# Kernel optimization log

Hardware: AMD Instinct MI355X
Metric: run time of the kernel (lower is better)

The kernel has to match this reference:

```python
import jax, jax.numpy as jnp
import numpy as np

BN_EPS = 1e-5


def _interpolate(xyz1, xyz2, points2):
    # squared pairwise distances [B, N, S]
    d = (jnp.sum(xyz1 ** 2, -1)[:, :, None]
         + jnp.sum(xyz2 ** 2, -1)[:, None, :]
         - 2.0 * jnp.einsum('bnc,bsc->bns', xyz1, xyz2))
    # 3 smallest distances (torch does a full sort; top-3 is the same math)
    neg_d, idx = jax.lax.top_k(-d, 3)          # [B, N, 3]
    dists = -neg_d
    w = 1.0 / (dists + 1e-8)
    w = w / jnp.sum(w, -1, keepdims=True)
    # gather points2 features at idx: [B, N, 3, D]
    gathered = jnp.take_along_axis(points2[:, None, :, :],
                                   idx[:, :, :, None], axis=2)
    return jnp.sum(gathered * w[:, :, :, None], axis=2)  # [B, N, D]


def _conv_bn_relu(x, w, b, gamma, beta):
    # x: [B, N, Cin]; 1x1 Conv1d == per-point dense layer
    y = jnp.einsum('bnc,oc->bno', x, w) + b
    mean = jnp.mean(y, axis=(0, 1))
    var = jnp.mean((y - mean) ** 2, axis=(0, 1))  # biased var (torch BN training)
    y = (y - mean) * jax.lax.rsqrt(var + BN_EPS) * gamma + beta
    return jax.nn.relu(y)


def setup_inputs() -> dict:
    key = jax.random.key(0)
    ks = jax.random.split(key, 8)
    B, N, S, D1, D2 = 8, 8192, 2048, 128, 256
    in_ch, mlp = D1 + D2, [256, 128]
    inp = {
        'xyz1': jax.random.normal(ks[0], (B, N, 3), jnp.float32),
        'xyz2': jax.random.normal(ks[1], (B, S, 3), jnp.float32),
        'points1': jax.random.normal(ks[2], (B, N, D1), jnp.float32),
        'points2': jax.random.normal(ks[3], (B, S, D2), jnp.float32),
    }
    c = in_ch
    for i, o in enumerate(mlp):
        kw = jax.random.fold_in(ks[4], i)
        inp[f'w{i}'] = jax.random.normal(kw, (o, c), jnp.float32) * (1.0 / np.sqrt(c))
        inp[f'b{i}'] = jnp.zeros((o,), jnp.float32)
        inp[f'g{i}'] = jnp.ones((o,), jnp.float32)
        inp[f'beta{i}'] = jnp.zeros((o,), jnp.float32)
        c = o
    return inp


def reference(xyz1, xyz2, points1, points2,
              w0, b0, g0, beta0, w1, b1, g1, beta1):
    interp = _interpolate(xyz1, xyz2, points2)          # [B, N, D2]
    x = jnp.concatenate([points1, interp], axis=-1)     # [B, N, D1+D2]
    x = _conv_bn_relu(x, w0, b0, g0, beta0)
    x = _conv_bn_relu(x, w1, b1, g1, beta1)
    return x                                            # [B, N, mlp[-1]]
```

## Files before the change

### kernel.cpp

```cpp
#include <hip/hip_runtime.h>
#include <hip/hip_bf16.h>

#define BATCH 8
#define NPTS  8192
#define SPTS  2048
#define D1C   128
#define D2C   256
#define C_IN  384
#define O0    256
#define O1    128
#define MROWS (BATCH * NPTS)
#define NCHUNK 8
#define CHSZ   256

typedef __attribute__((ext_vector_type(8))) short short8v;
typedef __attribute__((ext_vector_type(4))) float f32x4;

__device__ __forceinline__ unsigned short f2bf(float f) {
    union { float f; unsigned u; } v; v.f = f;
    unsigned u = v.u;
    return (unsigned short)((u + 0x7fffu + ((u >> 16) & 1u)) >> 16);
}
__device__ __forceinline__ float bf2f(unsigned short h) {
    union { unsigned u; float f; } v; v.u = ((unsigned)h) << 16;
    return v.f;
}
__device__ __forceinline__ void gload_lds16(const void* g, void* l) {
    __builtin_amdgcn_global_load_lds(
        (const __attribute__((address_space(1))) void*)g,
        (__attribute__((address_space(3))) void*)l, 16, 0, 0);
}

__global__ __launch_bounds__(256, 8) void nn3_scan(
    const float* __restrict__ xyz1, const float* __restrict__ xyz2,
    float* __restrict__ candD, int* __restrict__ candI)
{
    __shared__ float4 P[CHSZ];
    const int t  = threadIdx.x;
    const int qb = blockIdx.x;
    const int c  = blockIdx.y;
    const int b  = qb >> 5;

    {
        const float* src = xyz2 + ((size_t)b * SPTS + c * CHSZ) * 3;
        float px = src[t * 3 + 0];
        float py = src[t * 3 + 1];
        float pz = src[t * 3 + 2];
        P[t] = make_float4(px, py, pz, px * px + py * py + pz * pz);
    }
    __syncthreads();

    const int q = qb * 256 + t;
    const float* qp = xyz1 + (size_t)q * 3;
    const float qx = qp[0], qy = qp[1], qz = qp[2];
    const float qn = qx * qx + qy * qy + qz * qz;

    float d0 = 1e30f, d1 = 1e30f, d2 = 1e30f;
    int   i0 = 0,     i1 = 0,     i2 = 0;
    const int gbase = c * CHSZ;

    #pragma unroll 4
    for (int s = 0; s < CHSZ; ++s) {
        float4 p = P[s];
        float dot = qx * p.x + qy * p.y + qz * p.z;
        float d = (qn + p.w) - 2.0f * dot;
        bool c0 = d < d0, c1 = d < d1, c2 = d < d2;
        int gi = gbase + s;
        float t2 = __builtin_amdgcn_fmed3f(d, d1, d2);
        float t1 = __builtin_amdgcn_fmed3f(d, d0, d1);
        i2 = c1 ? i1 : (c2 ? gi : i2);
        i1 = c0 ? i0 : (c1 ? gi : i1);
        i0 = c0 ? gi : i0;
        d2 = t2; d1 = t1; d0 = fminf(d, d0);
    }

    const size_t base = (size_t)c * (MROWS * 3) + (size_t)q * 3;
    candD[base + 0] = d0; candD[base + 1] = d1; candD[base + 2] = d2;
    candI[base + 0] = i0; candI[base + 1] = i1; candI[base + 2] = i2;
}

__global__ __launch_bounds__(256) void nn3_merge(
    const float* __restrict__ candD, const int* __restrict__ candI,
    int* __restrict__ idx3, float* __restrict__ wgt3)
{
    const int q = blockIdx.x * 256 + threadIdx.x;

    float d0 = 1e30f, d1 = 1e30f, d2 = 1e30f;
    int   i0 = 0,     i1 = 0,     i2 = 0;

    #pragma unroll
    for (int c = 0; c < NCHUNK; ++c) {
        const size_t base = (size_t)c * (MROWS * 3) + (size_t)q * 3;
        #pragma unroll
        for (int j = 0; j < 3; ++j) {
            float d = candD[base + j];
            int  gi = candI[base + j];
            bool c0 = d < d0, c1 = d < d1, c2 = d < d2;
            float t2 = __builtin_amdgcn_fmed3f(d, d1, d2);
            float t1 = __builtin_amdgcn_fmed3f(d, d0, d1);
            i2 = c1 ? i1 : (c2 ? gi : i2);
            i1 = c0 ? i0 : (c1 ? gi : i1);
            i0 = c0 ? gi : i0;
            d2 = t2; d1 = t1; d0 = fminf(d, d0);
        }
    }

    float wa = 1.0f / (d0 + 1e-8f);
    float wb = 1.0f / (d1 + 1e-8f);
    float wc = 1.0f / (d2 + 1e-8f);
    float inv = 1.0f / (wa + wb + wc);
    wa *= inv; wb *= inv; wc *= inv;

    idx3[q * 3 + 0] = i0;
    idx3[q * 3 + 1] = i1;
    idx3[q * 3 + 2] = i2;
    wgt3[q * 3 + 0] = wa;
    wgt3[q * 3 + 1] = wb;
    wgt3[q * 3 + 2] = wc;
}

__global__ __launch_bounds__(256) void cvt_f32_bf16(
    const float* __restrict__ src, unsigned short* __restrict__ dst)
{
    int i = blockIdx.x * 256 + threadIdx.x;
    float4 v = ((const float4*)src)[i];
    ushort4 o;
    o.x = f2bf(v.x); o.y = f2bf(v.y); o.z = f2bf(v.z); o.w = f2bf(v.w);
    ((ushort4*)dst)[i] = o;
}

__global__ __launch_bounds__(256) void interp_kernel(
    const float* __restrict__ points2,
    const int* __restrict__ idx3, const float* __restrict__ wgt3,
    unsigned short* __restrict__ xI)
{
    const int w    = threadIdx.x >> 6;
    const int lane = threadIdx.x & 63;
    const int m    = blockIdx.x * 4 + w;
    const int b    = m >> 13;

    const float* p2b = points2 + (size_t)b * SPTS * D2C;
    const int  gi0 = idx3[m * 3 + 0];
    const int  gi1 = idx3[m * 3 + 1];
    const int  gi2 = idx3[m * 3 + 2];
    const float w0 = wgt3[m * 3 + 0];
    const float w1 = wgt3[m * 3 + 1];
    const float w2 = wgt3[m * 3 + 2];

    float4 a = *(const float4*)(p2b + (size_t)gi0 * D2C + lane * 4);
    float4 bb = *(const float4*)(p2b + (size_t)gi1 * D2C + lane * 4);
    float4 c = *(const float4*)(p2b + (size_t)gi2 * D2C + lane * 4);

    ushort4 o;
    o.x = f2bf(w0 * a.x + w1 * bb.x + w2 * c.x);
    o.y = f2bf(w0 * a.y + w1 * bb.y + w2 * c.y);
    o.z = f2bf(w0 * a.z + w1 * bb.z + w2 * c.z);
    o.w = f2bf(w0 * a.w + w1 * bb.w + w2 * c.w);
    *(ushort4*)(xI + (size_t)m * D2C + lane * 4) = o;
}

__global__ __launch_bounds__(512) void gemm0_mfma(
    const float* __restrict__ points1, const unsigned short* __restrict__ xI,
    const unsigned short* __restrict__ w0bf, const float* __restrict__ b0,
    unsigned short* __restrict__ y0bf,
    float* __restrict__ sum0, float* __restrict__ sq0)
{
    __shared__ __align__(16) unsigned short As[128 * 32];
    __shared__ __align__(16) unsigned short Bs[256 * 32];

    const int t    = threadIdx.x;
    const int lane = t & 63;
    const int w    = t >> 6;
    const int wm   = w >> 2;
    const int wn   = w & 3;
    const int rowBase = blockIdx.x * 128;

    const int r      = t >> 2;
    const int ks_log = (t & 3) ^ ((t >> 3) & 3);

    const float* p1row = points1 + (size_t)(rowBase + r) * D1C;
    const unsigned short* xrow = xI + (size_t)(rowBase + r) * D2C + ks_log * 8;
    unsigned short* asw = As + t * 8;
    char* ldsA = (char*)As + w * 1024;

    const unsigned short* gB0 = w0bf + (size_t)r * C_IN + ks_log * 8;
    const unsigned short* gB1 = w0bf + (size_t)(128 + r) * C_IN + ks_log * 8;
    char* ldsB0 = (char*)Bs + w * 1024;
    char* ldsB1 = (char*)Bs + 8192 + w * 1024;

    const int rp = (lane & 15) * 64 + (((lane >> 4) ^ ((lane >> 1) & 3)) * 16);
    const char* aBase = (const char*)As + (wm * 64) * 64 + rp;
    const char* bBase = (const char*)Bs + (wn * 64) * 64 + rp;

    f32x4 acc[4][4] = {};

    for (int kt = 0; kt < C_IN / 32; ++kt) {
        gload_lds16(gB0 + kt * 32, ldsB0);
        gload_lds16(gB1 + kt * 32, ldsB1);

        if (kt < 4) {
            const int k = kt * 32 + ks_log * 8;
            float4 f0 = *(const float4*)(p1row + k);
            float4 f1 = *(const float4*)(p1row + k + 4);
            short8v av;
            av[0] = (short)f2bf(f0.x); av[1] = (short)f2bf(f0.y);
            av[2] = (short)f2bf(f0.z); av[3] = (short)f2bf(f0.w);
            av[4] = (short)f2bf(f1.x); av[5] = (short)f2bf(f1.y);
            av[6] = (short)f2bf(f1.z); av[7] = (short)f2bf(f1.w);
            *(short8v*)asw = av;
        } else {
            gload_lds16(xrow + (kt - 4) * 32, ldsA);
        }

        __syncthreads();

        short8v a[4], bf[4];
        #pragma unroll
        for (int m = 0; m < 4; ++m) a[m]  = *(const short8v*)(aBase + m * 1024);
        #pragma unroll
        for (int n = 0; n < 4; ++n) bf[n] = *(const short8v*)(bBase + n * 1024);
        #pragma unroll
        for (int m = 0; m < 4; ++m)
            #pragma unroll
            for (int n = 0; n < 4; ++n)
                acc[m][n] = __builtin_amdgcn_mfma_f32_16x16x32_bf16(
                    a[m], bf[n], acc[m][n], 0, 0, 0);

        __syncthreads();
    }

    const int colw = wn * 64 + (lane & 15);
    const int rowE = rowBase + wm * 64 + ((lane >> 4) * 4);
    float bias[4];
    #pragma unroll
    for (int n = 0; n < 4; ++n) bias[n] = b0[colw + n * 16];

    float cs[4] = {0.f, 0.f, 0.f, 0.f}, cq[4] = {0.f, 0.f, 0.f, 0.f};
    #pragma unroll
    for (int m = 0; m < 4; ++m)
        #pragma unroll
        for (int n = 0; n < 4; ++n)
            #pragma unroll
            for (int j = 0; j < 4; ++j) {
                float v = acc[m][n][j] + bias[n];
                y0bf[(size_t)(rowE + m * 16 + j) * O0 + colw + n * 16] = f2bf(v);
                cs[n] += v; cq[n] += v * v;
            }

    #pragma unroll
    for (int n = 0; n < 4; ++n) {
        float s = cs[n], qv = cq[n];
        s  += __shfl_xor(s, 16);  s  += __shfl_xor(s, 32);
        qv += __shfl_xor(qv, 16); qv += __shfl_xor(qv, 32);
        if (lane < 16) {
            atomicAdd(&sum0[colw + n * 16], s);
            atomicAdd(&sq0[colw + n * 16], qv);
        }
    }
}

__global__ void stats_kernel(const float* __restrict__ sum, const float* __restrict__ sq,
                             const float* __restrict__ g, const float* __restrict__ beta,
                             float* __restrict__ scale, float* __restrict__ shift,
                             int C, float invM)
{
    int c = blockIdx.x * blockDim.x + threadIdx.x;
    if (c < C) {
        float mean = sum[c] * invM;
        float var  = sq[c] * invM - mean * mean;
        float s = g[c] * rsqrtf(var + 1e-5f);
        scale[c] = s;
        shift[c] = beta[c] - mean * s;
    }
}

__global__ __launch_bounds__(256) void gemm1_mfma(
    const unsigned short* __restrict__ x1, const unsigned short* __restrict__ w1bf,
    const float* __restrict__ scale0, const float* __restrict__ shift0,
    const float* __restrict__ b1, float* __restrict__ out,
    float* __restrict__ sum1, float* __restrict__ sq1)
{
    __shared__ __align__(16) unsigned short As[128 * 32];
    __shared__ __align__(16) unsigned short Bs[128 * 32];
    __shared__ float sc[O0], sh[O0];

    const int t    = threadIdx.x;
    const int lane = t & 63;
    const int w    = t >> 6;
    const int wm   = w >> 1, wn = w & 1;
    const int rowBase = blockIdx.x * 128;

    sc[t] = scale0[t];
    sh[t] = shift0[t];
    __syncthreads();

    const int r      = t >> 2;
    const int kl     = t & 3;
    const int kp     = kl ^ ((r >> 1) & 3);
    const int ks_log = kl ^ ((r >> 1) & 3);

    const unsigned short* gA0 = x1 + (size_t)(rowBase + r) * O0 + kl * 8;
    const unsigned short* gA1 = x1 + (size_t)(rowBase + 64 + r) * O0 + kl * 8;
    unsigned short* dA0 = As + r * 32 + kp * 8;
    unsigned short* dA1 = As + (64 + r) * 32 + kp * 8;

    const unsigned short* gB0 = w1bf + (size_t)r * O0 + ks_log * 8;
    const unsigned short* gB1 = w1bf + (size_t)(64 + r) * O0 + ks_log * 8;
    char* ldsB0 = (char*)Bs + w * 1024;
    char* ldsB1 = (char*)Bs + 4096 + w * 1024;

    const int rp = (lane & 15) * 64 + (((lane >> 4) ^ ((lane >> 1) & 3)) * 16);
    const char* aBase = (const char*)As + (wm * 64) * 64 + rp;
    const char* bBase = (const char*)Bs + (wn * 64) * 64 + rp;

    f32x4 acc[4][4] = {};

    for (int kt = 0; kt < O0 / 32; ++kt) {
        gload_lds16(gB0 + kt * 32, ldsB0);
        gload_lds16(gB1 + kt * 32, ldsB1);

        const int ch = kt * 32 + kl * 8;
        float4 s0v = *(const float4*)(sc + ch);
        float4 s1v = *(const float4*)(sc + ch + 4);
        float4 h0v = *(const float4*)(sh + ch);
        float4 h1v = *(const float4*)(sh + ch + 4);
        short8v v0 = *(const short8v*)(gA0 + kt * 32);
        short8v v1 = *(const short8v*)(gA1 + kt * 32);
        short8v o0, o1;
        o0[0] = (short)f2bf(fmaxf(0.f, bf2f((unsigned short)v0[0]) * s0v.x + h0v.x));
        o0[1] = (short)f2bf(fmaxf(0.f, bf2f((unsigned short)v0[1]) * s0v.y + h0v.y));
        o0[2] = (short)f2bf(fmaxf(0.f, bf2f((unsigned short)v0[2]) * s0v.z + h0v.z));
        o0[3] = (short)f2bf(fmaxf(0.f, bf2f((unsigned short)v0[3]) * s0v.w + h0v.w));
        o0[4] = (short)f2bf(fmaxf(0.f, bf2f((unsigned short)v0[4]) * s1v.x + h1v.x));
        o0[5] = (short)f2bf(fmaxf(0.f, bf2f((unsigned short)v0[5]) * s1v.y + h1v.y));
        o0[6] = (short)f2bf(fmaxf(0.f, bf2f((unsigned short)v0[6]) * s1v.z + h1v.z));
        o0[7] = (short)f2bf(fmaxf(0.f, bf2f((unsigned short)v0[7]) * s1v.w + h1v.w));
        o1[0] = (short)f2bf(fmaxf(0.f, bf2f((unsigned short)v1[0]) * s0v.x + h0v.x));
        o1[1] = (short)f2bf(fmaxf(0.f, bf2f((unsigned short)v1[1]) * s0v.y + h0v.y));
        o1[2] = (short)f2bf(fmaxf(0.f, bf2f((unsigned short)v1[2]) * s0v.z + h0v.z));
        o1[3] = (short)f2bf(fmaxf(0.f, bf2f((unsigned short)v1[3]) * s0v.w + h0v.w));
        o1[4] = (short)f2bf(fmaxf(0.f, bf2f((unsigned short)v1[4]) * s1v.x + h1v.x));
        o1[5] = (short)f2bf(fmaxf(0.f, bf2f((unsigned short)v1[5]) * s1v.y + h1v.y));
        o1[6] = (short)f2bf(fmaxf(0.f, bf2f((unsigned short)v1[6]) * s1v.z + h1v.z));
        o1[7] = (short)f2bf(fmaxf(0.f, bf2f((unsigned short)v1[7]) * s1v.w + h1v.w));
        *(short8v*)dA0 = o0;
        *(short8v*)dA1 = o1;

        __syncthreads();

        short8v a[4], bf[4];
        #pragma unroll
        for (int m = 0; m < 4; ++m) a[m]  = *(const short8v*)(aBase + m * 1024);
        #pragma unroll
        for (int n = 0; n < 4; ++n) bf[n] = *(const short8v*)(bBase + n * 1024);
        #pragma unroll
        for (int m = 0; m < 4; ++m)
            #pragma unroll
            for (int n = 0; n < 4; ++n)
                acc[m][n] = __builtin_amdgcn_mfma_f32_16x16x32_bf16(
                    a[m], bf[n], acc[m][n], 0, 0, 0);

        __syncthreads();
    }

    const int colw = wn * 64 + (lane & 15);
    const int rowE = rowBase + wm * 64 + ((lane >> 4) * 4);
    float bias[4];
    #pragma unroll
    for (int n = 0; n < 4; ++n) bias[n] = b1[colw + n * 16];

    float cs[4] = {0.f, 0.f, 0.f, 0.f}, cq[4] = {0.f, 0.f, 0.f, 0.f};
    #pragma unroll
    for (int m = 0; m < 4; ++m)
        #pragma unroll
        for (int n = 0; n < 4; ++n)
            #pragma unroll
            for (int j = 0; j < 4; ++j) {
                float v = acc[m][n][j] + bias[n];
                out[(size_t)(rowE + m * 16 + j) * O1 + colw + n * 16] = v;
                cs[n] += v; cq[n] += v * v;
            }

    #pragma unroll
    for (int n = 0; n < 4; ++n) {
        float s = cs[n], qv = cq[n];
        s  += __shfl_xor(s, 16);  s  += __shfl_xor(s, 32);
        qv += __shfl_xor(qv, 16); qv += __shfl_xor(qv, 32);
        if (lane < 16) {
            atomicAdd(&sum1[colw + n * 16], s);
            atomicAdd(&sq1[colw + n * 16], qv);
        }
    }
}

__global__ __launch_bounds__(256) void bn_relu_kernel(
    float* __restrict__ out,
    const float* __restrict__ scale, const float* __restrict__ shift)
{
    int i = blockIdx.x * blockDim.x + threadIdx.x;
    float4 v = ((float4*)out)[i];
    int c = (i * 4) & (O1 - 1);
    v.x = fmaxf(0.f, v.x * scale[c + 0] + shift[c + 0]);
    v.y = fmaxf(0.f, v.y * scale[c + 1] + shift[c + 1]);
    v.z = fmaxf(0.f, v.z * scale[c + 2] + shift[c + 2]);
    v.w = fmaxf(0.f, v.w * scale[c + 3] + shift[c + 3]);
    ((float4*)out)[i] = v;
}

extern "C" void kernel_launch(void* const* d_in, const int* in_sizes, int n_in,
                              void* d_out, int out_size, void* d_ws, size_t ws_size,
                              hipStream_t stream)
{
    const float* xyz1    = (const float*)d_in[0];
    const float* xyz2    = (const float*)d_in[1];
    const float* points1 = (const float*)d_in[2];
    const float* points2 = (const float*)d_in[3];
    const float* w0      = (const float*)d_in[4];
    const float* b0      = (const float*)d_in[5];
    const float* g0      = (const float*)d_in[6];
    const float* beta0   = (const float*)d_in[7];
    const float* w1      = (const float*)d_in[8];
    const float* b1      = (const float*)d_in[9];
    const float* g1      = (const float*)d_in[10];
    const float* beta1   = (const float*)d_in[11];

    float* wsf = (float*)d_ws;
    float* sum0   = wsf;
    float* sq0    = wsf + 256;
    float* sum1   = wsf + 512;
    float* sq1    = wsf + 640;
    float* scale0 = wsf + 768;
    float* shift0 = wsf + 1024;
    float* scale1 = wsf + 1280;
    float* shift1 = wsf + 1408;
    unsigned short* w0bf = (unsigned short*)(wsf + 1536);
    unsigned short* w1bf = (unsigned short*)(wsf + 50688);
    unsigned short* y0bf = (unsigned short*)(wsf + 67072);
    int*   idx3   = (int*)(wsf + 67072);
    float* wgt3   = wsf + 263680;
    float* candD  = wsf + 460288;
    int*   candI  = (int*)(wsf + 2033152);
    unsigned short* xI = (unsigned short*)(wsf + 8455680);

    hipMemsetAsync(d_ws, 0, 768 * sizeof(float), stream);

    cvt_f32_bf16<<<(O0 * C_IN / 4) / 256, 256, 0, stream>>>(w0, w0bf);
    cvt_f32_bf16<<<(O1 * O0 / 4) / 256, 256, 0, stream>>>(w1, w1bf);

    nn3_scan<<<dim3(MROWS / 256, NCHUNK), 256, 0, stream>>>(xyz1, xyz2, candD, candI);
    nn3_merge<<<MROWS / 256, 256, 0, stream>>>(candD, candI, idx3, wgt3);

    interp_kernel<<<MROWS / 4, 256, 0, stream>>>(points2, idx3, wgt3, xI);

    gemm0_mfma<<<MROWS / 128, 512, 0, stream>>>(
        points1, xI, w0bf, b0, y0bf, sum0, sq0);

    stats_kernel<<<1, 256, 0, stream>>>(sum0, sq0, g0, beta0, scale0, shift0,
                                        O0, 1.0f / MROWS);

    gemm1_mfma<<<MROWS / 128, 256, 0, stream>>>(
        y0bf, w1bf, scale0, shift0, b1, (float*)d_out, sum1, sq1);

    stats_kernel<<<1, 128, 0, stream>>>(sum1, sq1, g1, beta1, scale1, shift1,
                                        O1, 1.0f / MROWS);

    bn_relu_kernel<<<(out_size / 4) / 256, 256, 0, stream>>>(
        (float*)d_out, scale1, shift1);
}
```

Before: 196.2 us.

## Precompute padded xyz2 in global, scan without LDS, store gemm1 output as bf16

A small prep kernel turns xyz2 into float4 records (x, y, z, |p|^2) in global memory. The nearest-neighbour scan now reads these directly, which removes the LDS staging and block barrier, and its loop is unrolled by 8 instead of 4. The second GEMM writes a bf16 intermediate instead of the fp32 output, and the final BN+ReLU pass reads that bf16 buffer and writes fp32, halving the traffic of the intermediate read and write. The risks are broadcast global loads in the scan hot loop instead of LDS reads, an extra launch, and bf16 rounding before normalisation.

```diff
diff --git a/kernel.cpp b/kernel.cpp
--- a/kernel.cpp
+++ b/kernel.cpp
@@ -31,24 +31,26 @@
         (__attribute__((address_space(3))) void*)l, 16, 0, 0);
 }
 
+__global__ __launch_bounds__(256) void prep_p4(
+    const float* __restrict__ xyz2, float4* __restrict__ P4g)
+{
+    int i = blockIdx.x * 256 + threadIdx.x;
+    float px = xyz2[i * 3 + 0];
+    float py = xyz2[i * 3 + 1];
+    float pz = xyz2[i * 3 + 2];
+    P4g[i] = make_float4(px, py, pz, px * px + py * py + pz * pz);
+}
+
 __global__ __launch_bounds__(256, 8) void nn3_scan(
-    const float* __restrict__ xyz1, const float* __restrict__ xyz2,
+    const float* __restrict__ xyz1, const float4* __restrict__ P4g,
     float* __restrict__ candD, int* __restrict__ candI)
 {
-    __shared__ float4 P[CHSZ];
     const int t  = threadIdx.x;
     const int qb = blockIdx.x;
     const int c  = blockIdx.y;
     const int b  = qb >> 5;
 
-    {
-        const float* src = xyz2 + ((size_t)b * SPTS + c * CHSZ) * 3;
-        float px = src[t * 3 + 0];
-        float py = src[t * 3 + 1];
-        float pz = src[t * 3 + 2];
-        P[t] = make_float4(px, py, pz, px * px + py * py + pz * pz);
-    }
-    __syncthreads();
+    const float4* __restrict__ P = P4g + ((size_t)b * SPTS + c * CHSZ);
 
     const int q = qb * 256 + t;
     const float* qp = xyz1 + (size_t)q * 3;
@@ -59,7 +61,7 @@
     int   i0 = 0,     i1 = 0,     i2 = 0;
     const int gbase = c * CHSZ;
 
-    #pragma unroll 4
+    #pragma unroll 8
     for (int s = 0; s < CHSZ; ++s) {
         float4 p = P[s];
         float dot = qx * p.x + qy * p.y + qz * p.z;
@@ -277,7 +279,7 @@
 __global__ __launch_bounds__(256) void gemm1_mfma(
     const unsigned short* __restrict__ x1, const unsigned short* __restrict__ w1bf,
     const float* __restrict__ scale0, const float* __restrict__ shift0,
-    const float* __restrict__ b1, float* __restrict__ out,
+    const float* __restrict__ b1, unsigned short* __restrict__ y1bf,
     float* __restrict__ sum1, float* __restrict__ sq1)
 {
     __shared__ __align__(16) unsigned short As[128 * 32];
@@ -377,7 +379,7 @@
             #pragma unroll
             for (int j = 0; j < 4; ++j) {
                 float v = acc[m][n][j] + bias[n];
-                out[(size_t)(rowE + m * 16 + j) * O1 + colw + n * 16] = v;
+                y1bf[(size_t)(rowE + m * 16 + j) * O1 + colw + n * 16] = f2bf(v);
                 cs[n] += v; cq[n] += v * v;
             }
 
@@ -393,18 +395,28 @@
     }
 }
 
-__global__ __launch_bounds__(256) void bn_relu_kernel(
-    float* __restrict__ out,
+__global__ __launch_bounds__(256) void bn_relu_out(
+    const unsigned short* __restrict__ y1bf, float* __restrict__ out,
     const float* __restrict__ scale, const float* __restrict__ shift)
 {
-    int i = blockIdx.x * blockDim.x + threadIdx.x;
-    float4 v = ((float4*)out)[i];
-    int c = (i * 4) & (O1 - 1);
-    v.x = fmaxf(0.f, v.x * scale[c + 0] + shift[c + 0]);
-    v.y = fmaxf(0.f, v.y * scale[c + 1] + shift[c + 1]);
-    v.z = fmaxf(0.f, v.z * scale[c + 2] + shift[c + 2]);
-    v.w = fmaxf(0.f, v.w * scale[c + 3] + shift[c + 3]);
-    ((float4*)out)[i] = v;
+    int i = blockIdx.x * 256 + threadIdx.x;
+    short8v v = ((const short8v*)y1bf)[i];
+    int c = (i * 8) & (O1 - 1);
+    float4 sa = *(const float4*)(scale + c);
+    float4 sb = *(const float4*)(scale + c + 4);
+    float4 ha = *(const float4*)(shift + c);
+    float4 hb = *(const float4*)(shift + c + 4);
+    float4 o0, o1;
+    o0.x = fmaxf(0.f, bf2f((unsigned short)v[0]) * sa.x + ha.x);
+    o0.y = fmaxf(0.f, bf2f((unsigned short)v[1]) * sa.y + ha.y);
+    o0.z = fmaxf(0.f, bf2f((unsigned short)v[2]) * sa.z + ha.z);
+    o0.w = fmaxf(0.f, bf2f((unsigned short)v[3]) * sa.w + ha.w);
+    o1.x = fmaxf(0.f, bf2f((unsigned short)v[4]) * sb.x + hb.x);
+    o1.y = fmaxf(0.f, bf2f((unsigned short)v[5]) * sb.y + hb.y);
+    o1.z = fmaxf(0.f, bf2f((unsigned short)v[6]) * sb.z + hb.z);
+    o1.w = fmaxf(0.f, bf2f((unsigned short)v[7]) * sb.w + hb.w);
+    ((float4*)out)[i * 2 + 0] = o0;
+    ((float4*)out)[i * 2 + 1] = o1;
 }
 
 extern "C" void kernel_launch(void* const* d_in, const int* in_sizes, int n_in,
@@ -435,19 +447,23 @@
     float* shift1 = wsf + 1408;
     unsigned short* w0bf = (unsigned short*)(wsf + 1536);
     unsigned short* w1bf = (unsigned short*)(wsf + 50688);
+    float4* P4g   = (float4*)(wsf + 67072);
+    float*  candD = wsf + 132608;
+    int*    candI = (int*)(wsf + 1705472);
+    int*    idx3  = (int*)(wsf + 3278336);
+    float*  wgt3  = wsf + 3474944;
     unsigned short* y0bf = (unsigned short*)(wsf + 67072);
-    int*   idx3   = (int*)(wsf + 67072);
-    float* wgt3   = wsf + 263680;
-    float* candD  = wsf + 460288;
-    int*   candI  = (int*)(wsf + 2033152);
-    unsigned short* xI = (unsigned short*)(wsf + 8455680);
+    unsigned short* xI   = (unsigned short*)(wsf + 8455680);
+    unsigned short* y1bf = (unsigned short*)(wsf + 8455680);
 
     hipMemsetAsync(d_ws, 0, 768 * sizeof(float), stream);
 
     cvt_f32_bf16<<<(O0 * C_IN / 4) / 256, 256, 0, stream>>>(w0, w0bf);
     cvt_f32_bf16<<<(O1 * O0 / 4) / 256, 256, 0, stream>>>(w1, w1bf);
 
-    nn3_scan<<<dim3(MROWS / 256, NCHUNK), 256, 0, stream>>>(xyz1, xyz2, candD, candI);
+    prep_p4<<<(BATCH * SPTS) / 256, 256, 0, stream>>>(xyz2, P4g);
+
+    nn3_scan<<<dim3(MROWS / 256, NCHUNK), 256, 0, stream>>>(xyz1, P4g, candD, candI);
     nn3_merge<<<MROWS / 256, 256, 0, stream>>>(candD, candI, idx3, wgt3);
 
     interp_kernel<<<MROWS / 4, 256, 0, stream>>>(points2, idx3, wgt3, xI);
@@ -459,11 +475,11 @@
                                         O0, 1.0f / MROWS);
 
     gemm1_mfma<<<MROWS / 128, 256, 0, stream>>>(
-        y0bf, w1bf, scale0, shift0, b1, (float*)d_out, sum1, sq1);
+        y0bf, w1bf, scale0, shift0, b1, y1bf, sum1, sq1);
 
     stats_kernel<<<1, 128, 0, stream>>>(sum1, sq1, g1, beta1, scale1, shift1,
                                         O1, 1.0f / MROWS);
 
-    bn_relu_kernel<<<(out_size / 4) / 256, 256, 0, stream>>>(
-        (float*)d_out, scale1, shift1);
-}
+    bn_relu_out<<<(MROWS * O1 / 8) / 256, 256, 0, stream>>>(
+        y1bf, (float*)d_out, scale1, shift1);
+}
```

After: 202.1 us. 3.0% more time.

## Fuse BatchNorm stats and apply into GEMM epilogues via grid-wide barrier

Applied to the files above, without the earlier changes.

Both GEMM kernels now hold their accumulators in registers, wait at a software grid barrier until every block has added its column sums, then compute the BN scale and shift and write normalized, ReLU'd outputs directly. This removes the two stats kernels and the separate bn_relu pass, drops the fp32 round-trip of the final output, and lets gemm1 stream its already-normalized A operand straight into LDS with global_load_lds. The scheme relies on all 512 blocks being co-resident, which the launch bounds are meant to guarantee; otherwise the spin barrier deadlocks. It also adds spin-wait cost and register pressure from keeping accumulators live across the barrier.

```diff
diff --git a/kernel.cpp b/kernel.cpp
--- a/kernel.cpp
+++ b/kernel.cpp
@@ -12,6 +12,7 @@
 #define MROWS (BATCH * NPTS)
 #define NCHUNK 8
 #define CHSZ   256
+#define GRID_G 512
 
 typedef __attribute__((ext_vector_type(8))) short short8v;
 typedef __attribute__((ext_vector_type(4))) float f32x4;
@@ -29,6 +30,16 @@
     __builtin_amdgcn_global_load_lds(
         (const __attribute__((address_space(1))) void*)g,
         (__attribute__((address_space(3))) void*)l, 16, 0, 0);
+}
+
+__device__ __forceinline__ void grid_barrier(int* bar, int nblocks) {
+    __syncthreads();
+    if (threadIdx.x == 0) {
+        __threadfence();
+        atomicAdd(bar, 1);
+        while (atomicAdd(bar, 0) < nblocks) __builtin_amdgcn_s_sleep(2);
+    }
+    __syncthreads();
 }
 
 __global__ __launch_bounds__(256, 8) void nn3_scan(
@@ -159,11 +170,12 @@
     *(ushort4*)(xI + (size_t)m * D2C + lane * 4) = o;
 }
 
-__global__ __launch_bounds__(512) void gemm0_mfma(
+__global__ __launch_bounds__(512, 4) void gemm0_fused(
     const float* __restrict__ points1, const unsigned short* __restrict__ xI,
     const unsigned short* __restrict__ w0bf, const float* __restrict__ b0,
-    unsigned short* __restrict__ y0bf,
-    float* __restrict__ sum0, float* __restrict__ sq0)
+    const float* __restrict__ g0, const float* __restrict__ beta0,
+    unsigned short* __restrict__ x1,
+    float* __restrict__ sum0, float* __restrict__ sq0, int* __restrict__ bar)
 {
     __shared__ __align__(16) unsigned short As[128 * 32];
     __shared__ __align__(16) unsigned short Bs[256 * 32];
@@ -243,10 +255,8 @@
             #pragma unroll
             for (int j = 0; j < 4; ++j) {
                 float v = acc[m][n][j] + bias[n];
-                y0bf[(size_t)(rowE + m * 16 + j) * O0 + colw + n * 16] = f2bf(v);
                 cs[n] += v; cq[n] += v * v;
             }
-
     #pragma unroll
     for (int n = 0; n < 4; ++n) {
         float s = cs[n], qv = cq[n];
@@ -257,32 +267,37 @@
             atomicAdd(&sq0[colw + n * 16], qv);
         }
     }
-}
-
-__global__ void stats_kernel(const float* __restrict__ sum, const float* __restrict__ sq,
-                             const float* __restrict__ g, const float* __restrict__ beta,
-                             float* __restrict__ scale, float* __restrict__ shift,
-                             int C, float invM)
-{
-    int c = blockIdx.x * blockDim.x + threadIdx.x;
-    if (c < C) {
-        float mean = sum[c] * invM;
-        float var  = sq[c] * invM - mean * mean;
-        float s = g[c] * rsqrtf(var + 1e-5f);
-        scale[c] = s;
-        shift[c] = beta[c] - mean * s;
-    }
-}
-
-__global__ __launch_bounds__(256) void gemm1_mfma(
+
+    grid_barrier(bar, GRID_G);
+
+    const float invM = 1.0f / MROWS;
+    #pragma unroll
+    for (int n = 0; n < 4; ++n) {
+        const int c = colw + n * 16;
+        float sm = __hip_atomic_load(&sum0[c], __ATOMIC_RELAXED, __HIP_MEMORY_SCOPE_AGENT);
+        float sv = __hip_atomic_load(&sq0[c],  __ATOMIC_RELAXED, __HIP_MEMORY_SCOPE_AGENT);
+        float mean = sm * invM;
+        float var  = sv * invM - mean * mean;
+        float sc = g0[c] * rsqrtf(var + 1e-5f);
+        float sh = beta0[c] - mean * sc;
+        #pragma unroll
+        for (int m = 0; m < 4; ++m)
+            #pragma unroll
+            for (int j = 0; j < 4; ++j) {
+                float x = fmaxf(0.f, (acc[m][n][j] + bias[n]) * sc + sh);
+                x1[(size_t)(rowE + m * 16 + j) * O0 + c] = f2bf(x);
+            }
+    }
+}
+
+__global__ __launch_bounds__(256, 2) void gemm1_fused(
     const unsigned short* __restrict__ x1, const unsigned short* __restrict__ w1bf,
-    const float* __restrict__ scale0, const float* __restrict__ shift0,
-    const float* __restrict__ b1, float* __restrict__ out,
-    float* __restrict__ sum1, float* __restrict__ sq1)
+    const float* __restrict__ b1, const float* __restrict__ g1,
+    const float* __restrict__ beta1, float* __restrict__ out,
+    float* __restrict__ sum1, float* __restrict__ sq1, int* __restrict__ bar)
 {
     __shared__ __align__(16) unsigned short As[128 * 32];
     __shared__ __align__(16) unsigned short Bs[128 * 32];
-    __shared__ float sc[O0], sh[O0];
 
     const int t    = threadIdx.x;
     const int lane = t & 63;
@@ -290,22 +305,15 @@
     const int wm   = w >> 1, wn = w & 1;
     const int rowBase = blockIdx.x * 128;
 
-    sc[t] = scale0[t];
-    sh[t] = shift0[t];
-    __syncthreads();
-
     const int r      = t >> 2;
-    const int kl     = t & 3;
-    const int kp     = kl ^ ((r >> 1) & 3);
-    const int ks_log = kl ^ ((r >> 1) & 3);
-
-    const unsigned short* gA0 = x1 + (size_t)(rowBase + r) * O0 + kl * 8;
-    const unsigned short* gA1 = x1 + (size_t)(rowBase + 64 + r) * O0 + kl * 8;
-    unsigned short* dA0 = As + r * 32 + kp * 8;
-    unsigned short* dA1 = As + (64 + r) * 32 + kp * 8;
-
+    const int ks_log = (t & 3) ^ ((t >> 3) & 3);
+
+    const unsigned short* gA0 = x1 + (size_t)(rowBase + r) * O0 + ks_log * 8;
+    const unsigned short* gA1 = x1 + (size_t)(rowBase + 64 + r) * O0 + ks_log * 8;
     const unsigned short* gB0 = w1bf + (size_t)r * O0 + ks_log * 8;
     const unsigned short* gB1 = w1bf + (size_t)(64 + r) * O0 + ks_log * 8;
+    char* ldsA0 = (char*)As + w * 1024;
+    char* ldsA1 = (char*)As + 4096 + w * 1024;
     char* ldsB0 = (char*)Bs + w * 1024;
     char* ldsB1 = (char*)Bs + 4096 + w * 1024;
 
@@ -316,35 +324,10 @@
     f32x4 acc[4][4] = {};
 
     for (int kt = 0; kt < O0 / 32; ++kt) {
+        gload_lds16(gA0 + kt * 32, ldsA0);
+        gload_lds16(gA1 + kt * 32, ldsA1);
         gload_lds16(gB0 + kt * 32, ldsB0);
         gload_lds16(gB1 + kt * 32, ldsB1);
-
-        const int ch = kt * 32 + kl * 8;
-        float4 s0v = *(const float4*)(sc + ch);
-        float4 s1v = *(const float4*)(sc + ch + 4);
-        float4 h0v = *(const float4*)(sh + ch);
-        float4 h1v = *(const float4*)(sh + ch + 4);
-        short8v v0 = *(const short8v*)(gA0 + kt * 32);
-        short8v v1 = *(const short8v*)(gA1 + kt * 32);
-        short8v o0, o1;
-        o0[0] = (short)f2bf(fmaxf(0.f, bf2f((unsigned short)v0[0]) * s0v.x + h0v.x));
-        o0[1] = (short)f2bf(fmaxf(0.f, bf2f((unsigned short)v0[1]) * s0v.y + h0v.y));
-        o0[2] = (short)f2bf(fmaxf(0.f, bf2f((unsigned short)v0[2]) * s0v.z + h0v.z));
-        o0[3] = (short)f2bf(fmaxf(0.f, bf2f((unsigned short)v0[3]) * s0v.w + h0v.w));
-        o0[4] = (short)f2bf(fmaxf(0.f, bf2f((unsigned short)v0[4]) * s1v.x + h1v.x));
-        o0[5] = (short)f2bf(fmaxf(0.f, bf2f((unsigned short)v0[5]) * s1v.y + h1v.y));
-        o0[6] = (short)f2bf(fmaxf(0.f, bf2f((unsigned short)v0[6]) * s1v.z + h1v.z));
-        o0[7] = (short)f2bf(fmaxf(0.f, bf2f((unsigned short)v0[7]) * s1v.w + h1v.w));
-        o1[0] = (short)f2bf(fmaxf(0.f, bf2f((unsigned short)v1[0]) * s0v.x + h0v.x));
-        o1[1] = (short)f2bf(fmaxf(0.f, bf2f((unsigned short)v1[1]) * s0v.y + h0v.y));
-        o1[2] = (short)f2bf(fmaxf(0.f, bf2f((unsigned short)v1[2]) * s0v.z + h0v.z));
-        o1[3] = (short)f2bf(fmaxf(0.f, bf2f((unsigned short)v1[3]) * s0v.w + h0v.w));
-        o1[4] = (short)f2bf(fmaxf(0.f, bf2f((unsigned short)v1[4]) * s1v.x + h1v.x));
-        o1[5] = (short)f2bf(fmaxf(0.f, bf2f((unsigned short)v1[5]) * s1v.y + h1v.y));
-        o1[6] = (short)f2bf(fmaxf(0.f, bf2f((unsigned short)v1[6]) * s1v.z + h1v.z));
-        o1[7] = (short)f2bf(fmaxf(0.f, bf2f((unsigned short)v1[7]) * s1v.w + h1v.w));
-        *(short8v*)dA0 = o0;
-        *(short8v*)dA1 = o1;
 
         __syncthreads();
 
@@ -377,10 +360,8 @@
             #pragma unroll
             for (int j = 0; j < 4; ++j) {
                 float v = acc[m][n][j] + bias[n];
-                out[(size_t)(rowE + m * 16 + j) * O1 + colw + n * 16] = v;
                 cs[n] += v; cq[n] += v * v;
             }
-
     #pragma unroll
     for (int n = 0; n < 4; ++n) {
         float s = cs[n], qv = cq[n];
@@ -391,20 +372,27 @@
             atomicAdd(&sq1[colw + n * 16], qv);
         }
     }
-}
-
-__global__ __launch_bounds__(256) void bn_relu_kernel(
-    float* __restrict__ out,
-    const float* __restrict__ scale, const float* __restrict__ shift)
-{
-    int i = blockIdx.x * blockDim.x + threadIdx.x;
-    float4 v = ((float4*)out)[i];
-    int c = (i * 4) & (O1 - 1);
-    v.x = fmaxf(0.f, v.x * scale[c + 0] + shift[c + 0]);
-    v.y = fmaxf(0.f, v.y * scale[c + 1] + shift[c + 1]);
-    v.z = fmaxf(0.f, v.z * scale[c + 2] + shift[c + 2]);
-    v.w = fmaxf(0.f, v.w * scale[c + 3] + shift[c + 3]);
-    ((float4*)out)[i] = v;
+
+    grid_barrier(bar, GRID_G);
+
+    const float invM = 1.0f / MROWS;
+    #pragma unroll
+    for (int n = 0; n < 4; ++n) {
+        const int c = colw + n * 16;
+        float sm = __hip_atomic_load(&sum1[c], __ATOMIC_RELAXED, __HIP_MEMORY_SCOPE_AGENT);
+        float sv = __hip_atomic_load(&sq1[c],  __ATOMIC_RELAXED, __HIP_MEMORY_SCOPE_AGENT);
+        float mean = sm * invM;
+        float var  = sv * invM - mean * mean;
+        float sc = g1[c] * rsqrtf(var + 1e-5f);
+        float sh = beta1[c] - mean * sc;
+        #pragma unroll
+        for (int m = 0; m < 4; ++m)
+            #pragma unroll
+            for (int j = 0; j < 4; ++j) {
+                float v = fmaxf(0.f, (acc[m][n][j] + bias[n]) * sc + sh);
+                out[(size_t)(rowE + m * 16 + j) * O1 + c] = v;
+            }
+    }
 }
 
 extern "C" void kernel_launch(void* const* d_in, const int* in_sizes, int n_in,
@@ -425,24 +413,22 @@
     const float* beta1   = (const float*)d_in[11];
 
     float* wsf = (float*)d_ws;
-    float* sum0   = wsf;
-    float* sq0    = wsf + 256;
-    float* sum1   = wsf + 512;
-    float* sq1    = wsf + 640;
-    float* scale0 = wsf + 768;
-    float* shift0 = wsf + 1024;
-    float* scale1 = wsf + 1280;
-    float* shift1 = wsf + 1408;
+    float* sum0 = wsf;
+    float* sq0  = wsf + 256;
+    float* sum1 = wsf + 512;
+    float* sq1  = wsf + 640;
+    int*   bar0 = (int*)(wsf + 768);
+    int*   bar1 = (int*)(wsf + 769);
     unsigned short* w0bf = (unsigned short*)(wsf + 1536);
     unsigned short* w1bf = (unsigned short*)(wsf + 50688);
-    unsigned short* y0bf = (unsigned short*)(wsf + 67072);
-    int*   idx3   = (int*)(wsf + 67072);
-    float* wgt3   = wsf + 263680;
-    float* candD  = wsf + 460288;
-    int*   candI  = (int*)(wsf + 2033152);
+    float* candD = wsf + 67072;
+    int*   candI = (int*)(wsf + 1639936);
+    int*   idx3  = (int*)(wsf + 3212800);
+    float* wgt3  = wsf + 3409408;
+    unsigned short* x1 = (unsigned short*)(wsf + 67072);
     unsigned short* xI = (unsigned short*)(wsf + 8455680);
 
-    hipMemsetAsync(d_ws, 0, 768 * sizeof(float), stream);
+    hipMemsetAsync(d_ws, 0, 1024 * sizeof(float), stream);
 
     cvt_f32_bf16<<<(O0 * C_IN / 4) / 256, 256, 0, stream>>>(w0, w0bf);
     cvt_f32_bf16<<<(O1 * O0 / 4) / 256, 256, 0, stream>>>(w1, w1bf);
@@ -452,18 +438,9 @@
 
     interp_kernel<<<MROWS / 4, 256, 0, stream>>>(points2, idx3, wgt3, xI);
 
-    gemm0_mfma<<<MROWS / 128, 512, 0, stream>>>(
-        points1, xI, w0bf, b0, y0bf, sum0, sq0);
-
-    stats_kernel<<<1, 256, 0, stream>>>(sum0, sq0, g0, beta0, scale0, shift0,
-                                        O0, 1.0f / MROWS);
-
-    gemm1_mfma<<<MROWS / 128, 256, 0, stream>>>(
-        y0bf, w1bf, scale0, shift0, b1, (float*)d_out, sum1, sq1);
-
-    stats_kernel<<<1, 128, 0, stream>>>(sum1, sq1, g1, beta1, scale1, shift1,
-                                        O1, 1.0f / MROWS);
-
-    bn_relu_kernel<<<(out_size / 4) / 256, 256, 0, stream>>>(
-        (float*)d_out, scale1, shift1);
-}
+    gemm0_fused<<<GRID_G, 512, 0, stream>>>(
+        points1, xI, w0bf, b0, g0, beta0, x1, sum0, sq0, bar0);
+
+    gemm1_fused<<<GRID_G, 256, 0, stream>>>(
+        x1, w1bf, b1, g1, beta1, (float*)d_out, sum1, sq1, bar1);
+}
```

Result: slower. 250.6 us (+27.7%).
